# Optimization experiments

Hardware: AMD Instinct MI355X
Metric: run time of the kernel (lower is better)

## Reference

```python
import jax, jax.numpy as jnp
import numpy as np

DIM = 512
HEADS = 8
DIM_HEAD = 64
LANDMARKS = 256  # dim // 2
PINV_ITERS = 6
KERNEL = 33  # residual conv kernel
NUM_LAYERS = 2
NUM_CLASSES = 2


def layernorm(x, g, b, eps=1e-5):
    mu = x.mean(-1, keepdims=True)
    var = ((x - mu) ** 2).mean(-1, keepdims=True)
    return (x - mu) * jax.lax.rsqrt(var + eps) * g + b


def moore_penrose_pinv(x, iters=PINV_ITERS):
    # x: (b, h, m, m); scaling uses GLOBAL max over all batch/heads (torch.max)
    abs_x = jnp.abs(x)
    col = abs_x.sum(-1).max()
    row = abs_x.sum(-2).max()
    z = jnp.swapaxes(x, -1, -2) / (col * row)
    I = jnp.eye(x.shape[-1], dtype=x.dtype)
    for _ in range(iters):
        xz = x @ z
        z = 0.25 * z @ (13. * I - xz @ (15. * I - xz @ (7. * I - xz)))
    return z


def nystrom_attention(x, w_qkv, w_out, b_out, conv_w):
    # x: (b, n, dim)
    b, n, _ = x.shape
    m = LANDMARKS
    pad = (m - n % m) % m
    if pad:
        x = jnp.pad(x, ((0, 0), (pad, 0), (0, 0)))  # pad at FRONT
    nf = n + pad
    qkv = x @ w_qkv  # (b, nf, 3*h*dh)
    qkv = qkv.reshape(b, nf, 3, HEADS, DIM_HEAD)
    q = jnp.transpose(qkv[:, :, 0], (0, 2, 1, 3)) * (DIM_HEAD ** -0.5)  # (b,h,nf,dh)
    k = jnp.transpose(qkv[:, :, 1], (0, 2, 1, 3))
    v = jnp.transpose(qkv[:, :, 2], (0, 2, 1, 3))
    l = nf // m
    q_l = q.reshape(b, HEADS, m, l, DIM_HEAD).mean(3)  # (b,h,m,dh)
    k_l = k.reshape(b, HEADS, m, l, DIM_HEAD).mean(3)
    sim1 = jnp.einsum('bhid,bhjd->bhij', q, k_l)      # (b,h,nf,m)
    sim2 = jnp.einsum('bhid,bhjd->bhij', q_l, k_l)    # (b,h,m,m)
    sim3 = jnp.einsum('bhid,bhjd->bhij', q_l, k)      # (b,h,m,nf)
    attn1 = jax.nn.softmax(sim1, axis=-1)
    attn2 = jax.nn.softmax(sim2, axis=-1)
    attn3 = jax.nn.softmax(sim3, axis=-1)
    attn2_inv = moore_penrose_pinv(attn2)
    out = (attn1 @ attn2_inv) @ (attn3 @ v)  # (b,h,nf,dh)
    # residual depthwise conv over sequence dim, per head (Conv2d groups=heads)
    res = jax.lax.conv_general_dilated(
        v, conv_w, window_strides=(1, 1), padding=((KERNEL // 2, KERNEL // 2), (0, 0)),
        dimension_numbers=('NCHW', 'OIHW', 'NCHW'), feature_group_count=HEADS)
    out = out + res
    out = jnp.transpose(out, (0, 2, 1, 3)).reshape(b, nf, HEADS * DIM_HEAD)
    out = out @ w_out + b_out
    return out[:, -n:]


def setup_inputs() -> dict:
    key = jax.random.key(0)
    ks = jax.random.split(key, 16)
    B, N = 2, 8191
    s = 0.02
    inp = {
        'h': jax.random.normal(ks[0], (B, N, 1024), jnp.float32),
        'w1': jax.random.normal(ks[1], (1024, DIM), jnp.float32) * s,
        'b1': jnp.zeros((DIM,), jnp.float32),
        'cls_token': jax.random.normal(ks[2], (1, 1, DIM), jnp.float32),
        'ln_g': jnp.ones((NUM_LAYERS, DIM), jnp.float32),
        'ln_b': jnp.zeros((NUM_LAYERS, DIM), jnp.float32),
        'w_qkv': jax.random.normal(ks[3], (NUM_LAYERS, DIM, 3 * HEADS * DIM_HEAD), jnp.float32) * s,
        'w_out': jax.random.normal(ks[4], (NUM_LAYERS, HEADS * DIM_HEAD, DIM), jnp.float32) * s,
        'b_out': jnp.zeros((NUM_LAYERS, DIM), jnp.float32),
        'conv_w': jax.random.normal(ks[5], (NUM_LAYERS, HEADS, 1, KERNEL, 1), jnp.float32) * s,
        'fn_g': jnp.ones((DIM,), jnp.float32),
        'fn_b': jnp.zeros((DIM,), jnp.float32),
        'w2': jax.random.normal(ks[6], (DIM, NUM_CLASSES), jnp.float32) * s,
        'b2': jnp.zeros((NUM_CLASSES,), jnp.float32),
    }
    return inp


def reference(h, w1, b1, cls_token, ln_g, ln_b, w_qkv, w_out, b_out, conv_w, fn_g, fn_b, w2, b2):
    x = jax.nn.relu(h @ w1 + b1)  # (B,N,512)
    B = x.shape[0]
    cls = jnp.broadcast_to(cls_token, (B, 1, DIM))
    x = jnp.concatenate([cls, x], axis=1)  # (B, N+1, 512)
    for i in range(NUM_LAYERS):
        x = x + nystrom_attention(layernorm(x, ln_g[i], ln_b[i]), w_qkv[i], w_out[i], b_out[i], conv_w[i])
    x = layernorm(x, fn_g, fn_b)[:, 0]
    logits = x @ w2 + b2
    return logits
```

## Files before the change

### kernel.cpp

```cpp
#include <hip/hip_runtime.h>
#include <hip/hip_bf16.h>

#define DIM 512
#define HEADS 8
#define DH 64
#define LM 256
#define NF 8192
#define BHN 16

typedef __attribute__((ext_vector_type(8))) short short8;
typedef __attribute__((ext_vector_type(4))) float f32x4;

__device__ __forceinline__ float bf2f(unsigned short u) {
  return __uint_as_float((unsigned)u << 16);
}
__device__ __forceinline__ unsigned short f2bf(float x) {
  unsigned u = __float_as_uint(x);
  unsigned r = u + 0x7fffu + ((u >> 16) & 1u);
  return (unsigned short)(r >> 16);
}

__device__ __forceinline__ void gl2lds16(const void* g, void* l) {
  __builtin_amdgcn_global_load_lds(
      (const __attribute__((address_space(1))) void*)g,
      (__attribute__((address_space(3))) void*)l, 16, 0, 0);
}

__device__ __forceinline__ float waveReduceSum(float v) {
#pragma unroll
  for (int o = 1; o < 64; o <<= 1) v += __shfl_xor(v, o);
  return v;
}
__device__ __forceinline__ float waveReduceMax(float v) {
#pragma unroll
  for (int o = 1; o < 64; o <<= 1) v = fmaxf(v, __shfl_xor(v, o));
  return v;
}
__device__ __forceinline__ float blockReduceSum256(float v, float* sm) {
  v = waveReduceSum(v);
  int w = threadIdx.x >> 6;
  __syncthreads();
  if ((threadIdx.x & 63) == 0) sm[w] = v;
  __syncthreads();
  return sm[0] + sm[1] + sm[2] + sm[3];
}
__device__ __forceinline__ float blockReduceMax256(float v, float* sm) {
  v = waveReduceMax(v);
  int w = threadIdx.x >> 6;
  __syncthreads();
  if ((threadIdx.x & 63) == 0) sm[w] = v;
  __syncthreads();
  return fmaxf(fmaxf(sm[0], sm[1]), fmaxf(sm[2], sm[3]));
}

__global__ __launch_bounds__(256)
void cvt_bf16(const float* __restrict__ in, unsigned short* __restrict__ out,
              long long n) {
  long long i = ((long long)blockIdx.x * 256 + threadIdx.x) * 4;
  if (i + 3 < n) {
    float4 v = *(const float4*)&in[i];
    ushort4 o;
    o.x = f2bf(v.x); o.y = f2bf(v.y); o.z = f2bf(v.z); o.w = f2bf(v.w);
    *(ushort4*)&out[i] = o;
  } else {
    for (; i < n; i++) out[i] = f2bf(in[i]);
  }
}

__global__ __launch_bounds__(256)
void cvt_transpose(const float* __restrict__ in, unsigned short* __restrict__ out,
                   int Kd, int Nd) {
  __shared__ float t[32][33];
  int x = threadIdx.x & 31, y = threadIdx.x >> 5;
#pragma unroll
  for (int i = 0; i < 32; i += 8) {
    int k = blockIdx.y * 32 + y + i, n = blockIdx.x * 32 + x;
    t[y + i][x] = in[(long long)k * Nd + n];
  }
  __syncthreads();
#pragma unroll
  for (int i = 0; i < 32; i += 8) {
    int n = blockIdx.x * 32 + y + i, k = blockIdx.y * 32 + x;
    out[(long long)n * Kd + k] = f2bf(t[x][y + i]);
  }
}

__global__ __launch_bounds__(256)
void vt_transpose(const unsigned short* __restrict__ VB,
                  unsigned short* __restrict__ VT) {
  __shared__ unsigned short t[64][80];
  int bh = blockIdx.x >> 7, tile = blockIdx.x & 127;
  int n0 = tile * 64;
  int tid = threadIdx.x;
#pragma unroll
  for (int it = 0; it < 2; it++) {
    int s = it * 256 + tid;
    int nl = s >> 3, sg = s & 7;
    *(short8*)&t[nl][sg * 8] =
        *(const short8*)&VB[((long long)bh * NF + n0 + nl) * DH + sg * 8];
  }
  __syncthreads();
#pragma unroll
  for (int it = 0; it < 2; it++) {
    int s = it * 256 + tid;
    int dl = s >> 3, sg = s & 7;
    short8 v;
#pragma unroll
    for (int j = 0; j < 8; j++) ((unsigned short*)&v)[j] = t[sg * 8 + j][dl];
    *(short8*)&VT[((long long)bh * DH + dl) * NF + n0 + sg * 8] = v;
  }
}

__global__ __launch_bounds__(256) void zero_f(float* __restrict__ p, int n) {
  int i = blockIdx.x * 256 + threadIdx.x;
  if (i < n) p[i] = 0.f;
}

__global__ __launch_bounds__(256) void write_cls(const float* __restrict__ cls,
                                                 float* __restrict__ X) {
  int t = blockIdx.x * 256 + threadIdx.x;
  int b = t >> 9, c = t & 511;
  X[(long long)b * NF * DIM + c] = cls[c];
}

#define MG_RELU 1
#define MG_ADDC 2
#define MG_BIAS 4
__global__ __launch_bounds__(256)
void gemm_mfma(const unsigned short* __restrict__ A,
               const unsigned short* __restrict__ B,
               const float* __restrict__ bias, float* __restrict__ C,
               unsigned short* __restrict__ qkv, unsigned short* __restrict__ vbuf,
               int M, int N, int K, int flags, int remap) {
  __shared__ short8 smem[1024];
  short8 (*Als)[64] = (short8 (*)[64])smem;
  short8 (*Bls)[64] = (short8 (*)[64])(smem + 512);
  const int tid = threadIdx.x;
  const int lane = tid & 63, wave = tid >> 6;
  const int wm = wave >> 1, wn = wave & 1;
  const int m0 = blockIdx.y * 128, n0 = blockIdx.x * 128;
  const int r16 = lane & 15, quad = lane >> 4;
  const unsigned short* pa0 = A + (long long)(m0 + 32 * wave + r16) * K + quad * 8;
  const unsigned short* pa1 = A + (long long)(m0 + 32 * wave + 16 + r16) * K + quad * 8;
  const unsigned short* pb0 = B + (long long)(n0 + 32 * wave + r16) * K + quad * 8;
  const unsigned short* pb1 = B + (long long)(n0 + 32 * wave + 16 + r16) * K + quad * 8;
  f32x4 acc[4][4] = {};
  for (int k0 = 0; k0 < K; k0 += 32) {
    gl2lds16(pa0, &Als[2 * wave][0]);
    gl2lds16(pa1, &Als[2 * wave + 1][0]);
    gl2lds16(pb0, &Bls[2 * wave][0]);
    gl2lds16(pb1, &Bls[2 * wave + 1][0]);
    pa0 += 32; pa1 += 32; pb0 += 32; pb1 += 32;
    __syncthreads();
    short8 af[4], bfr[4];
#pragma unroll
    for (int mt = 0; mt < 4; mt++) af[mt] = Als[wm * 4 + mt][lane];
#pragma unroll
    for (int nt = 0; nt < 4; nt++) bfr[nt] = Bls[wn * 4 + nt][lane];
#pragma unroll
    for (int mt = 0; mt < 4; mt++)
#pragma unroll
      for (int nt = 0; nt < 4; nt++)
        acc[mt][nt] = __builtin_amdgcn_mfma_f32_16x16x32_bf16(
            af[mt], bfr[nt], acc[mt][nt], 0, 0, 0);
    __syncthreads();
  }
  if (remap == 2) {
    unsigned short (*Ep)[32][64] = (unsigned short (*)[32][64])smem;
    int gn_base = n0 + wn * 64;
    int s = gn_base >> 9, hh = (gn_base >> 6) & 7;
    float scale = (s == 0) ? 0.125f : 1.f;
    unsigned short* basep =
        (s == 0) ? qkv : (s == 1) ? qkv + (long long)BHN * NF * DH : vbuf;
#pragma unroll
    for (int half = 0; half < 2; half++) {
      __builtin_amdgcn_s_waitcnt(0);
#pragma unroll
      for (int mt = half * 2; mt < half * 2 + 2; mt++)
#pragma unroll
        for (int nt = 0; nt < 4; nt++)
#pragma unroll
          for (int r = 0; r < 4; r++)
            Ep[wave][(mt & 1) * 16 + quad * 4 + r][nt * 16 + r16] =
                f2bf(acc[mt][nt][r] * scale);
      __builtin_amdgcn_s_waitcnt(0);
#pragma unroll
      for (int it = 0; it < 4; it++) {
        int idx = it * 64 + lane;
        int m_l = idx >> 3, sg = idx & 7;
        int gm = m0 + wm * 64 + half * 32 + m_l;
        int b = gm >> 13, n = gm & (NF - 1);
        int bh = b * HEADS + hh;
        short8 v = *(short8*)&Ep[wave][m_l][sg * 8];
        *(short8*)&basep[((long long)bh * NF + n) * DH + sg * 8] = v;
      }
    }
  } else {
#pragma unroll
    for (int mt = 0; mt < 4; mt++) {
#pragma unroll
      for (int nt = 0; nt < 4; nt++) {
#pragma unroll
        for (int r = 0; r < 4; r++) {
          int gm = m0 + wm * 64 + mt * 16 + quad * 4 + r;
          int gn = n0 + wn * 64 + nt * 16 + r16;
          if (gm >= M) continue;
          float v = acc[mt][nt][r];
          if (flags & MG_BIAS) v += bias[gn];
          long long idx;
          if (remap == 1) {
            int b = gm / 8191;
            int n = gm - b * 8191;
            idx = ((long long)(b * NF + 1 + n)) * DIM + gn;
          } else {
            idx = (long long)gm * N + gn;
          }
          if (flags & MG_ADDC) v += C[idx];
          if (flags & MG_RELU) v = fmaxf(v, 0.f);
          C[idx] = v;
        }
      }
    }
  }
}

__global__ __launch_bounds__(256)
void flash_attn1(const unsigned short* __restrict__ QB,
                 const unsigned short* __restrict__ KLB,
                 const unsigned short* __restrict__ WmB,
                 const unsigned short* __restrict__ XNC,
                 unsigned short* __restrict__ XNB2) {
  __shared__ unsigned short Plds[4][16][264];
  const int bh = blockIdx.y, b = bh >> 3, hh = bh & 7;
  const int tid = threadIdx.x, lane = tid & 63, wave = tid >> 6;
  const int r16 = lane & 15, quad = lane >> 4;
  const int m0w = blockIdx.x * 64 + wave * 16;
  const unsigned short* Aq = QB + (long long)bh * NF * DH;
  const unsigned short* Bk = KLB + (long long)bh * LM * DH;
  short8 af[2];
#pragma unroll
  for (int kc = 0; kc < 2; kc++)
    af[kc] = *(const short8*)&Aq[(long long)(m0w + r16) * DH + kc * 32 + quad * 8];
  f32x4 S[16] = {};
#pragma unroll
  for (int nt = 0; nt < 16; nt++) {
#pragma unroll
    for (int kc = 0; kc < 2; kc++) {
      short8 bb = *(const short8*)&Bk[(long long)(nt * 16 + r16) * DH + kc * 32 + quad * 8];
      S[nt] = __builtin_amdgcn_mfma_f32_16x16x32_bf16(af[kc], bb, S[nt], 0, 0, 0);
    }
  }
  float inv[4];
#pragma unroll
  for (int r = 0; r < 4; r++) {
    float m_ = S[0][r];
#pragma unroll
    for (int nt = 1; nt < 16; nt++) m_ = fmaxf(m_, S[nt][r]);
#pragma unroll
    for (int o = 1; o < 16; o <<= 1) m_ = fmaxf(m_, __shfl_xor(m_, o));
    float s_ = 0.f;
#pragma unroll
    for (int nt = 0; nt < 16; nt++) {
      float e = __expf(S[nt][r] - m_);
      S[nt][r] = e;
      s_ += e;
    }
#pragma unroll
    for (int o = 1; o < 16; o <<= 1) s_ += __shfl_xor(s_, o);
    inv[r] = 1.f / s_;
  }
#pragma unroll
  for (int nt = 0; nt < 16; nt++)
#pragma unroll
    for (int r = 0; r < 4; r++)
      Plds[wave][quad * 4 + r][nt * 16 + r16] = f2bf(S[nt][r] * inv[r]);
  __builtin_amdgcn_s_waitcnt(0);
  f32x4 O[4] = {};
#pragma unroll
  for (int kc = 0; kc < 8; kc++) {
    short8 a = *(short8*)&Plds[wave][r16][kc * 32 + quad * 8];
#pragma unroll
    for (int nt2 = 0; nt2 < 4; nt2++) {
      short8 bb = *(const short8*)&WmB[((long long)bh * DH + nt2 * 16 + r16) * LM +
                                       kc * 32 + quad * 8];
      O[nt2] = __builtin_amdgcn_mfma_f32_16x16x32_bf16(a, bb, O[nt2], 0, 0, 0);
    }
  }
#pragma unroll
  for (int nt2 = 0; nt2 < 4; nt2++)
#pragma unroll
    for (int r = 0; r < 4; r++) {
      int row = m0w + quad * 4 + r;
      int d = nt2 * 16 + r16;
      long long gi = ((long long)(b * NF + row)) * DIM + hh * DH + d;
      XNB2[gi] = f2bf(O[nt2][r] + bf2f(XNC[gi]));
    }
}

__global__ __launch_bounds__(256)
void flash_attn3(const unsigned short* __restrict__ QLB,
                 const unsigned short* __restrict__ KB,
                 const unsigned short* __restrict__ VT,
                 float* __restrict__ Opart, float* __restrict__ Mpart,
                 float* __restrict__ Lpart) {
  __shared__ unsigned short Plds[4][16][136];
  const int bh = blockIdx.z, ks = blockIdx.y;
  const int tid = threadIdx.x, lane = tid & 63, wave = tid >> 6;
  const int r16 = lane & 15, quad = lane >> 4;
  const int m0w = blockIdx.x * 64 + wave * 16;
  const unsigned short* Aq = QLB + (long long)bh * LM * DH;
  const unsigned short* Bk = KB + (long long)bh * NF * DH;
  const unsigned short* Vt = VT + (long long)bh * DH * NF;
  short8 af[2];
#pragma unroll
  for (int kc = 0; kc < 2; kc++)
    af[kc] = *(const short8*)&Aq[(long long)(m0w + r16) * DH + kc * 32 + quad * 8];
  f32x4 O[4] = {};
  float rm[4] = {-1e30f, -1e30f, -1e30f, -1e30f};
  float rl[4] = {};
  for (int t = 0; t < 4; t++) {
    int kv0 = ks * 512 + t * 128;
    f32x4 S[8] = {};
#pragma unroll
    for (int nt = 0; nt < 8; nt++) {
#pragma unroll
      for (int kc = 0; kc < 2; kc++) {
        short8 bb = *(const short8*)&Bk[(long long)(kv0 + nt * 16 + r16) * DH +
                                        kc * 32 + quad * 8];
        S[nt] = __builtin_amdgcn_mfma_f32_16x16x32_bf16(af[kc], bb, S[nt], 0, 0, 0);
      }
    }
#pragma unroll
    for (int r = 0; r < 4; r++) {
      float mt = S[0][r];
#pragma unroll
      for (int nt = 1; nt < 8; nt++) mt = fmaxf(mt, S[nt][r]);
#pragma unroll
      for (int o = 1; o < 16; o <<= 1) mt = fmaxf(mt, __shfl_xor(mt, o));
      float nm = fmaxf(rm[r], mt);
      float al = __expf(rm[r] - nm);
      rm[r] = nm;
      float s_ = 0.f;
#pragma unroll
      for (int nt = 0; nt < 8; nt++) {
        float e = __expf(S[nt][r] - nm);
        S[nt][r] = e;
        s_ += e;
      }
#pragma unroll
      for (int o = 1; o < 16; o <<= 1) s_ += __shfl_xor(s_, o);
      rl[r] = rl[r] * al + s_;
#pragma unroll
      for (int nt2 = 0; nt2 < 4; nt2++) O[nt2][r] *= al;
    }
#pragma unroll
    for (int nt = 0; nt < 8; nt++)
#pragma unroll
      for (int r = 0; r < 4; r++)
        Plds[wave][quad * 4 + r][nt * 16 + r16] = f2bf(S[nt][r]);
    __builtin_amdgcn_s_waitcnt(0);
#pragma unroll
    for (int kc2 = 0; kc2 < 4; kc2++) {
      short8 a = *(short8*)&Plds[wave][r16][kc2 * 32 + quad * 8];
#pragma unroll
      for (int nt2 = 0; nt2 < 4; nt2++) {
        short8 bb = *(const short8*)&Vt[(long long)(nt2 * 16 + r16) * NF + kv0 +
                                        kc2 * 32 + quad * 8];
        O[nt2] = __builtin_amdgcn_mfma_f32_16x16x32_bf16(a, bb, O[nt2], 0, 0, 0);
      }
    }
  }
  float* Ob = Opart + (((long long)ks * BHN + bh) * LM) * DH;
#pragma unroll
  for (int nt2 = 0; nt2 < 4; nt2++)
#pragma unroll
    for (int r = 0; r < 4; r++) {
      int row = m0w + quad * 4 + r;
      Ob[(long long)row * DH + nt2 * 16 + r16] = O[nt2][r];
    }
  if (r16 == 0) {
#pragma unroll
    for (int r = 0; r < 4; r++) {
      int row = m0w + quad * 4 + r;
      Mpart[((long long)ks * BHN + bh) * LM + row] = rm[r];
      Lpart[((long long)ks * BHN + bh) * LM + row] = rl[r];
    }
  }
}

__global__ __launch_bounds__(256)
void attn3_merge(const float* __restrict__ Opart, const float* __restrict__ Mpart,
                 const float* __restrict__ Lpart, float* __restrict__ O3) {
  int idx = blockIdx.x * 256 + threadIdx.x;
  int bh = idx >> 14, rem = idx & 16383;
  int row = rem >> 6, d = rem & 63;
  float mg = -1e30f;
#pragma unroll
  for (int c = 0; c < 16; c++)
    mg = fmaxf(mg, Mpart[((long long)c * BHN + bh) * LM + row]);
  float L = 0.f, acc = 0.f;
#pragma unroll
  for (int c = 0; c < 16; c++) {
    float e = __expf(Mpart[((long long)c * BHN + bh) * LM + row] - mg);
    L += Lpart[((long long)c * BHN + bh) * LM + row] * e;
    acc += Opart[(((long long)c * BHN + bh) * LM + row) * DH + d] * e;
  }
  O3[((long long)bh * LM + row) * DH + d] = acc / L;
}

__global__ __launch_bounds__(256)
void zinit(const float* __restrict__ a2, const unsigned* __restrict__ red,
           unsigned short* __restrict__ zn, unsigned short* __restrict__ zt) {
  float scale = 1.0f / __uint_as_float(red[1]);
  long long idx = (long long)blockIdx.x * 256 + threadIdx.x;
  int bh = (int)(idx >> 16);
  int ij = (int)(idx & 65535);
  int i = ij >> 8, j = ij & 255;
  zn[idx] = f2bf(a2[((long long)bh << 16) + (j << 8) + i] * scale);
  zt[idx] = f2bf(a2[idx] * scale);
}

#define PV_CN 1
#define PV_CT 2
#define PV_CF 4
#define PV_ID 8
__global__ __launch_bounds__(256)
void pinv_bf(const unsigned short* __restrict__ An,
             const unsigned short* __restrict__ Bt,
             unsigned short* __restrict__ Cn, unsigned short* __restrict__ Ct,
             float* __restrict__ Cf, float alpha, float ident, float beta,
             int flags) {
  __shared__ unsigned short Als[64][256];
  __shared__ unsigned short Bls[64][256];
  const int batch = blockIdx.z;
  An += (long long)batch * 65536;
  Bt += (long long)batch * 65536;
  const int tid = threadIdx.x, lane = tid & 63, wave = tid >> 6;
  const int wm2 = wave >> 1, wn2 = wave & 1;
  const int m0 = blockIdx.y * 64, n0 = blockIdx.x * 64;
  const int r16 = lane & 15, quad = lane >> 4;
#pragma unroll
  for (int j = 0; j < 8; j++) {
    int g = (j * 4 + wave) * 64 + lane;
    int row = g >> 5, plog = (g & 31) ^ (row & 7);
    gl2lds16(An + ((m0 + row) << 8) + plog * 8,
             (char*)Als + (j * 4 + wave) * 1024);
    gl2lds16(Bt + ((n0 + row) << 8) + plog * 8,
             (char*)Bls + (j * 4 + wave) * 1024);
  }
  __syncthreads();
  f32x4 acc[2][2] = {};
  const int arow0 = wm2 * 32 + r16, brow0 = wn2 * 32 + r16;
#pragma unroll
  for (int kk = 0; kk < 8; kk++) {
    short8 af[2], bfr[2];
#pragma unroll
    for (int mt = 0; mt < 2; mt++) {
      int row = arow0 + mt * 16;
      af[mt] = *(const short8*)((const char*)Als + row * 512 +
                                ((kk * 4 + quad) ^ (row & 7)) * 16);
    }
#pragma unroll
    for (int nt = 0; nt < 2; nt++) {
      int row = brow0 + nt * 16;
      bfr[nt] = *(const short8*)((const char*)Bls + row * 512 +
                                 ((kk * 4 + quad) ^ (row & 7)) * 16);
    }
#pragma unroll
    for (int mt = 0; mt < 2; mt++)
#pragma unroll
      for (int nt = 0; nt < 2; nt++)
        acc[mt][nt] = __builtin_amdgcn_mfma_f32_16x16x32_bf16(
            af[mt], bfr[nt], acc[mt][nt], 0, 0, 0);
  }
  long long cb = (long long)batch * 65536;
#pragma unroll
  for (int mt = 0; mt < 2; mt++) {
#pragma unroll
    for (int nt = 0; nt < 2; nt++) {
      int ncol = n0 + wn2 * 32 + nt * 16 + r16;
      float vals[4];
#pragma unroll
      for (int r = 0; r < 4; r++) {
        int mrow = wm2 * 32 + mt * 16 + quad * 4 + r;
        float v = beta * acc[mt][nt][r];
        if (flags & PV_ID) {
          unsigned short a = *(const unsigned short*)(
              (const char*)Als + mrow * 512 +
              (((ncol >> 3) ^ (mrow & 7)) * 16) + (ncol & 7) * 2);
          v += ident * bf2f(a);
        }
        vals[r] = v * alpha;
        int gm = m0 + mrow;
        if (flags & PV_CN) Cn[cb + ((long long)gm << 8) + ncol] = f2bf(vals[r]);
        if (flags & PV_CF) Cf[cb + ((long long)gm << 8) + ncol] = vals[r];
      }
      if (flags & PV_CT) {
        ushort4 o;
        o.x = f2bf(vals[0]); o.y = f2bf(vals[1]);
        o.z = f2bf(vals[2]); o.w = f2bf(vals[3]);
        *(ushort4*)&Ct[cb + ((long long)ncol << 8) + m0 + wm2 * 32 + mt * 16 +
                       quad * 4] = o;
      }
    }
  }
}

#define BG_BIDENT 16
__global__ __launch_bounds__(256)
void bgemm(const float* __restrict__ A, const float* __restrict__ B,
           float* __restrict__ C, int M, int N, int K,
           long long sA, long long sB, long long sC,
           float alpha, float ident, int flags) {
  const int batch = blockIdx.z;
  A += (long long)batch * sA;
  B += (long long)batch * sB;
  float* Cb = C + (long long)batch * sC;
  __shared__ float As[16][68];
  __shared__ float Bs[16][68];
  const int tid = threadIdx.x;
  const int tx = tid & 15, ty = tid >> 4;
  const int m0 = blockIdx.y * 64, n0 = blockIdx.x * 64;
  float acc[4][4] = {};
  for (int k0 = 0; k0 < K; k0 += 16) {
    {
      int k = tid & 15;
      int mBase = tid >> 4;
#pragma unroll
      for (int i = 0; i < 4; i++) {
        int m = mBase + i * 16;
        int gm = m0 + m;
        As[k][m] = (gm < M) ? A[(long long)gm * K + (k0 + k)] : 0.f;
      }
    }
    {
      int n = tid & 63;
      int kBase = tid >> 6;
#pragma unroll
      for (int i = 0; i < 4; i++) {
        int k = kBase + i * 4;
        int gn = n0 + n;
        float vb = (gn < N) ? B[(long long)(k0 + k) * N + gn] : 0.f;
        if (flags & BG_BIDENT) vb = ident * ((k0 + k) == gn ? 1.f : 0.f) - vb;
        Bs[k][n] = vb;
      }
    }
    __syncthreads();
#pragma unroll
    for (int k = 0; k < 16; k++) {
      float a[4], b[4];
#pragma unroll
      for (int i = 0; i < 4; i++) a[i] = As[k][ty * 4 + i];
#pragma unroll
      for (int j = 0; j < 4; j++) b[j] = Bs[k][tx * 4 + j];
#pragma unroll
      for (int i = 0; i < 4; i++)
#pragma unroll
        for (int j = 0; j < 4; j++) acc[i][j] = fmaf(a[i], b[j], acc[i][j]);
    }
    __syncthreads();
  }
#pragma unroll
  for (int i = 0; i < 4; i++) {
    int gm = m0 + ty * 4 + i;
    if (gm >= M) continue;
#pragma unroll
    for (int j = 0; j < 4; j++) {
      int gn = n0 + tx * 4 + j;
      if (gn >= N) continue;
      Cb[(long long)gm * N + gn] = alpha * acc[i][j];
    }
  }
}

__global__ __launch_bounds__(256)
void wm_gemm(const float* __restrict__ Z, const float* __restrict__ O3,
             unsigned short* __restrict__ WmT) {
  const int batch = blockIdx.y;
  const int m0 = blockIdx.x * 64;
  const float* A = Z + (long long)batch * 65536;
  const float* B = O3 + (long long)batch * LM * DH;
  __shared__ float As[16][68];
  __shared__ float Bs[16][68];
  const int tid = threadIdx.x, tx = tid & 15, ty = tid >> 4;
  float acc[4][4] = {};
  for (int k0 = 0; k0 < 256; k0 += 16) {
    {
      int k = tid & 15, mB = tid >> 4;
#pragma unroll
      for (int i = 0; i < 4; i++) {
        int m = mB + i * 16;
        As[k][m] = A[(long long)(m0 + m) * 256 + k0 + k];
      }
    }
    {
      int n = tid & 63, kB = tid >> 6;
#pragma unroll
      for (int i = 0; i < 4; i++) {
        int k = kB + i * 4;
        Bs[k][n] = B[(long long)(k0 + k) * DH + n];
      }
    }
    __syncthreads();
#pragma unroll
    for (int k = 0; k < 16; k++) {
      float a[4], b[4];
#pragma unroll
      for (int i = 0; i < 4; i++) a[i] = As[k][ty * 4 + i];
#pragma unroll
      for (int j = 0; j < 4; j++) b[j] = Bs[k][tx * 4 + j];
#pragma unroll
      for (int i = 0; i < 4; i++)
#pragma unroll
        for (int j = 0; j < 4; j++) acc[i][j] = fmaf(a[i], b[j], acc[i][j]);
    }
    __syncthreads();
  }
#pragma unroll
  for (int i = 0; i < 4; i++)
#pragma unroll
    for (int j = 0; j < 4; j++)
      WmT[((long long)batch * DH + tx * 4 + j) * LM + m0 + ty * 4 + i] =
          f2bf(acc[i][j]);
}

__global__ __launch_bounds__(256)
void layernorm_rows_bf16(const float* __restrict__ X, const float* __restrict__ g,
                         const float* __restrict__ bt,
                         unsigned short* __restrict__ Y) {
  __shared__ float sm[4];
  long long r = blockIdx.x;
  const float* x = X + r * DIM;
  int t = threadIdx.x;
  float v0 = x[t], v1 = x[t + 256];
  float mu = blockReduceSum256(v0 + v1, sm) * (1.f / DIM);
  float d0 = v0 - mu, d1 = v1 - mu;
  float var = blockReduceSum256(d0 * d0 + d1 * d1, sm) * (1.f / DIM);
  float rs = 1.0f / sqrtf(var + 1e-5f);
  unsigned short* y = Y + r * DIM;
  y[t] = f2bf(d0 * rs * g[t] + bt[t]);
  y[t + 256] = f2bf(d1 * rs * g[t + 256] + bt[t + 256]);
}

__global__ __launch_bounds__(64)
void landmarks_k(const unsigned short* __restrict__ q,
                 const unsigned short* __restrict__ k,
                 float* __restrict__ ql, float* __restrict__ kl,
                 unsigned short* __restrict__ qlb,
                 unsigned short* __restrict__ klb) {
  int bh = blockIdx.x >> 8, i = blockIdx.x & 255, d = threadIdx.x;
  long long base = ((long long)bh * NF + i * 32) * DH + d;
  float sq = 0.f, sk = 0.f;
#pragma unroll 4
  for (int l = 0; l < 32; l++) {
    sq += bf2f(q[base + (long long)l * DH]);
    sk += bf2f(k[base + (long long)l * DH]);
  }
  long long o = ((long long)bh * LM + i) * DH + d;
  float mq = sq * (1.f / 32.f), mk = sk * (1.f / 32.f);
  ql[o] = mq; kl[o] = mk;
  qlb[o] = f2bf(mq); klb[o] = f2bf(mk);
}

__global__ __launch_bounds__(256)
void sim2_softmax(const float* __restrict__ ql, const float* __restrict__ kl,
                  float* __restrict__ a2, unsigned short* __restrict__ a2b) {
  __shared__ float qs[64];
  __shared__ float sm[4];
  int bh = blockIdx.x >> 8, i = blockIdx.x & 255, t = threadIdx.x;
  if (t < 64) qs[t] = ql[((long long)bh * LM + i) * DH + t];
  __syncthreads();
  const float* krow = kl + (long long)bh * LM * DH + (long long)t * DH;
  float s = 0.f;
#pragma unroll
  for (int d = 0; d < 64; d++) s += qs[d] * krow[d];
  float m = blockReduceMax256(s, sm);
  float e = expf(s - m);
  float sum = blockReduceSum256(e, sm);
  long long off = ((long long)bh * LM + i) * LM + t;
  float v = e / sum;
  a2[off] = v;
  a2b[off] = f2bf(v);
}

__global__ __launch_bounds__(256)
void pinv_reduce(const float* __restrict__ a2, unsigned* __restrict__ red) {
  __shared__ float sm[4];
  int bh = blockIdx.x, t = threadIdx.x;
  const float* A = a2 + (long long)bh * LM * LM;
  float cs = 0.f;
  for (int i = 0; i < 256; i++) cs += fabsf(A[i * 256 + t]);
  float cm = blockReduceMax256(cs, sm);
  if (t == 0) atomicMax(&red[1], __float_as_uint(cm));
}

__global__ __launch_bounds__(256)
void conv_res_bf16(const unsigned short* __restrict__ vt,
                   const float* __restrict__ cw,
                   unsigned short* __restrict__ out) {
  int bh = blockIdx.x >> 6, tile = blockIdx.x & 63;
  int b = bh >> 3, hh = bh & 7;
  int t = threadIdx.x;
  int d = t & 63, pg = t >> 6;
  float wr[33];
#pragma unroll
  for (int kk = 0; kk < 33; kk++) wr[kk] = cw[hh * 33 + kk];
  const unsigned short* src = &vt[((long long)bh * DH + d) * NF];
  int base = tile * 128 + pg * 32;
  int n0 = base - 16;
  float win[64];
#pragma unroll
  for (int jj = 0; jj < 8; jj++) {
    int c = n0 + jj * 8;
    if (c >= 0 && c + 7 < NF) {
      short8 v = *(const short8*)&src[c];
#pragma unroll
      for (int j = 0; j < 8; j++)
        win[jj * 8 + j] = bf2f((unsigned short)v[j]);
    } else {
#pragma unroll
      for (int j = 0; j < 8; j++) {
        int nn = c + j;
        win[jj * 8 + j] = (nn >= 0 && nn < NF) ? bf2f(src[nn]) : 0.f;
      }
    }
  }
  unsigned short* dst = &out[((long long)(b * NF + base)) * DIM + hh * DH + d];
#pragma unroll
  for (int p = 0; p < 32; p++) {
    float s = 0.f;
#pragma unroll
    for (int kk = 0; kk < 33; kk++) s = fmaf(wr[kk], win[p + kk], s);
    dst[(long long)p * DIM] = f2bf(s);
  }
}

__global__ __launch_bounds__(256)
void final_head(const float* __restrict__ X, const float* __restrict__ g,
                const float* __restrict__ bt, const float* __restrict__ w2,
                const float* __restrict__ b2, float* __restrict__ out) {
  __shared__ float sm[4];
  int b = blockIdx.x, t = threadIdx.x;
  const float* row = X + (long long)b * NF * DIM;
  float v0 = row[t], v1 = row[t + 256];
  float mu = blockReduceSum256(v0 + v1, sm) * (1.f / DIM);
  float d0 = v0 - mu, d1 = v1 - mu;
  float var = blockReduceSum256(d0 * d0 + d1 * d1, sm) * (1.f / DIM);
  float rs = 1.0f / sqrtf(var + 1e-5f);
  float y0 = d0 * rs * g[t] + bt[t];
  float y1 = d1 * rs * g[t + 256] + bt[t + 256];
  float l0 = y0 * w2[t * 2 + 0] + y1 * w2[(t + 256) * 2 + 0];
  float l1 = y0 * w2[t * 2 + 1] + y1 * w2[(t + 256) * 2 + 1];
  l0 = blockReduceSum256(l0, sm);
  l1 = blockReduceSum256(l1, sm);
  if (t == 0) {
    out[b * 2 + 0] = l0 + b2[0];
    out[b * 2 + 1] = l1 + b2[1];
  }
}

extern "C" void kernel_launch(void* const* d_in, const int* in_sizes, int n_in,
                              void* d_out, int out_size, void* d_ws,
                              size_t ws_size, hipStream_t stream) {
  const float* h      = (const float*)d_in[0];
  const float* w1     = (const float*)d_in[1];
  const float* b1     = (const float*)d_in[2];
  const float* cls    = (const float*)d_in[3];
  const float* ln_g   = (const float*)d_in[4];
  const float* ln_b   = (const float*)d_in[5];
  const float* w_qkv  = (const float*)d_in[6];
  const float* w_out  = (const float*)d_in[7];
  const float* b_out  = (const float*)d_in[8];
  const float* conv_w = (const float*)d_in[9];
  const float* fn_g   = (const float*)d_in[10];
  const float* fn_b   = (const float*)d_in[11];
  const float* w2     = (const float*)d_in[12];
  const float* b2     = (const float*)d_in[13];

  float* ws = (float*)d_ws;
  const long long XSZ = (long long)2 * NF * DIM;
  const long long QSZ = (long long)BHN * NF * DH;
  float* X  = ws;
  unsigned short* STAGE = (unsigned short*)(X + XSZ);
  unsigned short* HB   = STAGE;
  unsigned short* XNB1 = STAGE;
  unsigned short* XNB2 = STAGE;
  unsigned short* VB   = STAGE + XSZ;
  unsigned short* XNC  = STAGE + XSZ;
  unsigned short* QB = STAGE + 2 * XSZ;
  unsigned short* KB = QB + QSZ;
  unsigned short* VT = KB + QSZ;
  float* QL = (float*)(VT + QSZ);
  float* KL = QL + 262144;
  unsigned short* QLB = (unsigned short*)(KL + 262144);
  unsigned short* KLB = QLB + 262144;
  float* A2 = (float*)(KLB + 262144);
  float* ZA = A2 + 1048576;
  float* ZB = ZA + 1048576;
  float* P  = ZB + 1048576;
  float* T1 = P + 1048576;
  float* T2 = T1 + 1048576;
  float* Mpart = T2 + 1048576;
  float* Lpart = Mpart + 65536;
  float* O3 = Lpart + 65536;
  unsigned short* WmB = (unsigned short*)(O3 + 262144);
  unsigned* RED = (unsigned*)(WmB + 262144);
  unsigned short* WT = (unsigned short*)(RED + 4);
  unsigned short* W1T = WT;
  unsigned short* WQ0 = W1T + 524288;
  unsigned short* WQ1 = WQ0 + 786432;
  unsigned short* WO0 = WQ1 + 786432;
  unsigned short* WO1 = WO0 + 262144;

  unsigned short* A2B = VB;
  float* Opart = (float*)VB;
  unsigned short* Zan = (unsigned short*)P;
  unsigned short* Zat = Zan + 1048576;
  unsigned short* Zbn = (unsigned short*)ZB;
  unsigned short* Zbt = Zbn + 1048576;
  unsigned short* Pn  = (unsigned short*)T1;
  unsigned short* Pt  = Pn + 1048576;
  unsigned short* T1t = (unsigned short*)T2;
  unsigned short* T2t = T1t + 1048576;

  write_cls<<<4, 256, 0, stream>>>(cls, X);
  cvt_bf16<<<16382, 256, 0, stream>>>(h, HB, (long long)16382 * 1024);
  cvt_transpose<<<dim3(512 / 32, 1024 / 32), 256, 0, stream>>>(w1, W1T, 1024, 512);
  cvt_transpose<<<dim3(1536 / 32, 512 / 32), 256, 0, stream>>>(w_qkv, WQ0, 512, 1536);
  cvt_transpose<<<dim3(1536 / 32, 512 / 32), 256, 0, stream>>>(
      w_qkv + (long long)DIM * 1536, WQ1, 512, 1536);
  cvt_transpose<<<dim3(512 / 32, 512 / 32), 256, 0, stream>>>(w_out, WO0, 512, 512);
  cvt_transpose<<<dim3(512 / 32, 512 / 32), 256, 0, stream>>>(
      w_out + (long long)DIM * DIM, WO1, 512, 512);
  gemm_mfma<<<dim3(4, 128), 256, 0, stream>>>(HB, W1T, b1, X, nullptr, nullptr,
                                              16382, 512, 1024, MG_RELU | MG_BIAS, 1);

  for (int L = 0; L < 2; L++) {
    layernorm_rows_bf16<<<2 * NF, 256, 0, stream>>>(X, ln_g + L * DIM,
                                                    ln_b + L * DIM, XNB1);
    gemm_mfma<<<dim3(12, 128), 256, 0, stream>>>(XNB1, L ? WQ1 : WQ0, nullptr,
                                                 nullptr, QB, VB, 16384, 1536,
                                                 512, 0, 2);
    vt_transpose<<<BHN * 128, 256, 0, stream>>>(VB, VT);

    landmarks_k<<<BHN * LM, 64, 0, stream>>>(QB, KB, QL, KL, QLB, KLB);
    sim2_softmax<<<BHN * LM, 256, 0, stream>>>(QL, KL, A2, A2B);
    zero_f<<<1, 256, 0, stream>>>((float*)RED, 4);
    pinv_reduce<<<BHN, 256, 0, stream>>>(A2, RED);
    zinit<<<4096, 256, 0, stream>>>(A2, RED, Zan, Zat);
    for (int it = 0; it < 5; it++) {
      const unsigned short* zcn = (it & 1) ? Zbn : Zan;
      const unsigned short* zct = (it & 1) ? Zbt : Zat;
      unsigned short* znn = (it & 1) ? Zan : Zbn;
      unsigned short* znt = (it & 1) ? Zat : Zbt;
      pinv_bf<<<dim3(4, 4, BHN), 256, 0, stream>>>(
          A2B, zct, Pn, Pt, nullptr, 1.f, 0.f, 1.f, PV_CN | PV_CT);
      pinv_bf<<<dim3(4, 4, BHN), 256, 0, stream>>>(
          Pn, Pt, nullptr, T1t, nullptr, 1.f, 7.f, -1.f, PV_CT | PV_ID);
      pinv_bf<<<dim3(4, 4, BHN), 256, 0, stream>>>(
          Pn, T1t, nullptr, T2t, nullptr, 1.f, 15.f, -1.f, PV_CT | PV_ID);
      if (it < 4)
        pinv_bf<<<dim3(4, 4, BHN), 256, 0, stream>>>(
            zcn, T2t, znn, znt, nullptr, 0.25f, 13.f, -1.f,
            PV_CN | PV_CT | PV_ID);
      else
        pinv_bf<<<dim3(4, 4, BHN), 256, 0, stream>>>(
            zcn, T2t, nullptr, nullptr, ZB, 0.25f, 13.f, -1.f, PV_CF | PV_ID);
    }
    bgemm<<<dim3(4, 4, BHN), 256, 0, stream>>>(A2, ZB, P, 256, 256, 256,
                                               65536, 65536, 65536, 1.f, 0.f, 0);
    bgemm<<<dim3(4, 4, BHN), 256, 0, stream>>>(P, P, T1, 256, 256, 256,
                                               65536, 65536, 65536, 1.f, 7.f,
                                               BG_BIDENT);
    bgemm<<<dim3(4, 4, BHN), 256, 0, stream>>>(P, T1, T2, 256, 256, 256,
                                               65536, 65536, 65536, 1.f, 15.f,
                                               BG_BIDENT);
    bgemm<<<dim3(4, 4, BHN), 256, 0, stream>>>(ZB, T2, ZA, 256, 256, 256,
                                               65536, 65536, 65536, 0.25f,
                                               13.f, BG_BIDENT);

    flash_attn3<<<dim3(4, 16, BHN), 256, 0, stream>>>(QLB, KB, VT, Opart, Mpart,
                                                      Lpart);
    attn3_merge<<<1024, 256, 0, stream>>>(Opart, Mpart, Lpart, O3);

    wm_gemm<<<dim3(4, BHN), 256, 0, stream>>>(ZA, O3, WmB);

    conv_res_bf16<<<BHN * 64, 256, 0, stream>>>(VT, conv_w + L * 264, XNC);

    flash_attn1<<<dim3(128, BHN), 256, 0, stream>>>(QB, KLB, WmB, XNC, XNB2);

    gemm_mfma<<<dim3(4, 128), 256, 0, stream>>>(XNB2, L ? WO1 : WO0,
                                                b_out + L * DIM, X, nullptr,
                                                nullptr, 16384, 512, 512,
                                                MG_ADDC | MG_BIAS, 0);
  }
  final_head<<<2, 256, 0, stream>>>(X, fn_g, fn_b, w2, b2, (float*)d_out);
}
```

Before: 1.440 ms.

## Shrink pinv tiles to 32x32, halve attn1 LDS staging, add MFMA priority hints

The pinv_bf batched GEMM now uses 32x32 output tiles with one MFMA accumulator per wave, launched on an 8x8 grid, giving four times as many blocks for the small 256x256 per-head matmuls. Each block also stages only 32 rows of A and B in LDS. flash_attn1 writes the softmax probabilities to LDS in two halves of 128 columns, halving its shared buffer. s_setprio is raised around the MFMA loops in both attention kernels. The aim is more occupancy and parallelism for the pinv chain and better interleaving of matrix and other work. The cost is less data reuse per block in pinv and an extra wait/LDS round in attn1.

```diff
diff --git a/kernel.cpp b/kernel.cpp
--- a/kernel.cpp
+++ b/kernel.cpp
@@ -230,7 +230,7 @@
                  const unsigned short* __restrict__ WmB,
                  const unsigned short* __restrict__ XNC,
                  unsigned short* __restrict__ XNB2) {
-  __shared__ unsigned short Plds[4][16][264];
+  __shared__ unsigned short Plds[4][16][136];
   const int bh = blockIdx.y, b = bh >> 3, hh = bh & 7;
   const int tid = threadIdx.x, lane = tid & 63, wave = tid >> 6;
   const int r16 = lane & 15, quad = lane >> 4;
@@ -242,6 +242,7 @@
   for (int kc = 0; kc < 2; kc++)
     af[kc] = *(const short8*)&Aq[(long long)(m0w + r16) * DH + kc * 32 + quad * 8];
   f32x4 S[16] = {};
+  __builtin_amdgcn_s_setprio(1);
 #pragma unroll
   for (int nt = 0; nt < 16; nt++) {
 #pragma unroll
@@ -250,6 +251,7 @@
       S[nt] = __builtin_amdgcn_mfma_f32_16x16x32_bf16(af[kc], bb, S[nt], 0, 0, 0);
     }
   }
+  __builtin_amdgcn_s_setprio(0);
   float inv[4];
 #pragma unroll
   for (int r = 0; r < 4; r++) {
@@ -269,22 +271,28 @@
     for (int o = 1; o < 16; o <<= 1) s_ += __shfl_xor(s_, o);
     inv[r] = 1.f / s_;
   }
-#pragma unroll
-  for (int nt = 0; nt < 16; nt++)
-#pragma unroll
-    for (int r = 0; r < 4; r++)
-      Plds[wave][quad * 4 + r][nt * 16 + r16] = f2bf(S[nt][r] * inv[r]);
-  __builtin_amdgcn_s_waitcnt(0);
   f32x4 O[4] = {};
 #pragma unroll
-  for (int kc = 0; kc < 8; kc++) {
-    short8 a = *(short8*)&Plds[wave][r16][kc * 32 + quad * 8];
-#pragma unroll
-    for (int nt2 = 0; nt2 < 4; nt2++) {
-      short8 bb = *(const short8*)&WmB[((long long)bh * DH + nt2 * 16 + r16) * LM +
-                                       kc * 32 + quad * 8];
-      O[nt2] = __builtin_amdgcn_mfma_f32_16x16x32_bf16(a, bb, O[nt2], 0, 0, 0);
-    }
+  for (int half = 0; half < 2; half++) {
+#pragma unroll
+    for (int nt = 0; nt < 8; nt++)
+#pragma unroll
+      for (int r = 0; r < 4; r++)
+        Plds[wave][quad * 4 + r][nt * 16 + r16] =
+            f2bf(S[half * 8 + nt][r] * inv[r]);
+    __builtin_amdgcn_s_waitcnt(0);
+    __builtin_amdgcn_s_setprio(1);
+#pragma unroll
+    for (int kc = 0; kc < 4; kc++) {
+      short8 a = *(short8*)&Plds[wave][r16][kc * 32 + quad * 8];
+#pragma unroll
+      for (int nt2 = 0; nt2 < 4; nt2++) {
+        short8 bb = *(const short8*)&WmB[((long long)bh * DH + nt2 * 16 + r16) * LM +
+                                         half * 128 + kc * 32 + quad * 8];
+        O[nt2] = __builtin_amdgcn_mfma_f32_16x16x32_bf16(a, bb, O[nt2], 0, 0, 0);
+      }
+    }
+    __builtin_amdgcn_s_setprio(0);
   }
 #pragma unroll
   for (int nt2 = 0; nt2 < 4; nt2++)
@@ -321,6 +329,7 @@
   for (int t = 0; t < 4; t++) {
     int kv0 = ks * 512 + t * 128;
     f32x4 S[8] = {};
+    __builtin_amdgcn_s_setprio(1);
 #pragma unroll
     for (int nt = 0; nt < 8; nt++) {
 #pragma unroll
@@ -330,6 +339,7 @@
         S[nt] = __builtin_amdgcn_mfma_f32_16x16x32_bf16(af[kc], bb, S[nt], 0, 0, 0);
       }
     }
+    __builtin_amdgcn_s_setprio(0);
 #pragma unroll
     for (int r = 0; r < 4; r++) {
       float mt = S[0][r];
@@ -359,6 +369,7 @@
       for (int r = 0; r < 4; r++)
         Plds[wave][quad * 4 + r][nt * 16 + r16] = f2bf(S[nt][r]);
     __builtin_amdgcn_s_waitcnt(0);
+    __builtin_amdgcn_s_setprio(1);
 #pragma unroll
     for (int kc2 = 0; kc2 < 4; kc2++) {
       short8 a = *(short8*)&Plds[wave][r16][kc2 * 32 + quad * 8];
@@ -369,6 +380,7 @@
         O[nt2] = __builtin_amdgcn_mfma_f32_16x16x32_bf16(a, bb, O[nt2], 0, 0, 0);
       }
     }
+    __builtin_amdgcn_s_setprio(0);
   }
   float* Ob = Opart + (((long long)ks * BHN + bh) * LM) * DH;
 #pragma unroll
@@ -430,17 +442,17 @@
              unsigned short* __restrict__ Cn, unsigned short* __restrict__ Ct,
              float* __restrict__ Cf, float alpha, float ident, float beta,
              int flags) {
-  __shared__ unsigned short Als[64][256];
-  __shared__ unsigned short Bls[64][256];
+  __shared__ unsigned short Als[32][256];
+  __shared__ unsigned short Bls[32][256];
   const int batch = blockIdx.z;
   An += (long long)batch * 65536;
   Bt += (long long)batch * 65536;
   const int tid = threadIdx.x, lane = tid & 63, wave = tid >> 6;
   const int wm2 = wave >> 1, wn2 = wave & 1;
-  const int m0 = blockIdx.y * 64, n0 = blockIdx.x * 64;
+  const int m0 = blockIdx.y * 32, n0 = blockIdx.x * 32;
   const int r16 = lane & 15, quad = lane >> 4;
 #pragma unroll
-  for (int j = 0; j < 8; j++) {
+  for (int j = 0; j < 4; j++) {
     int g = (j * 4 + wave) * 64 + lane;
     int row = g >> 5, plog = (g & 31) ^ (row & 7);
     gl2lds16(An + ((m0 + row) << 8) + plog * 8,
@@ -449,60 +461,39 @@
              (char*)Bls + (j * 4 + wave) * 1024);
   }
   __syncthreads();
-  f32x4 acc[2][2] = {};
-  const int arow0 = wm2 * 32 + r16, brow0 = wn2 * 32 + r16;
+  f32x4 acc = {};
+  const int arow = wm2 * 16 + r16, brow = wn2 * 16 + r16;
 #pragma unroll
   for (int kk = 0; kk < 8; kk++) {
-    short8 af[2], bfr[2];
-#pragma unroll
-    for (int mt = 0; mt < 2; mt++) {
-      int row = arow0 + mt * 16;
-      af[mt] = *(const short8*)((const char*)Als + row * 512 +
-                                ((kk * 4 + quad) ^ (row & 7)) * 16);
-    }
-#pragma unroll
-    for (int nt = 0; nt < 2; nt++) {
-      int row = brow0 + nt * 16;
-      bfr[nt] = *(const short8*)((const char*)Bls + row * 512 +
-                                 ((kk * 4 + quad) ^ (row & 7)) * 16);
-    }
-#pragma unroll
-    for (int mt = 0; mt < 2; mt++)
-#pragma unroll
-      for (int nt = 0; nt < 2; nt++)
-        acc[mt][nt] = __builtin_amdgcn_mfma_f32_16x16x32_bf16(
-            af[mt], bfr[nt], acc[mt][nt], 0, 0, 0);
+    short8 af = *(const short8*)((const char*)Als + arow * 512 +
+                                 ((kk * 4 + quad) ^ (arow & 7)) * 16);
+    short8 bfr = *(const short8*)((const char*)Bls + brow * 512 +
+                                  ((kk * 4 + quad) ^ (brow & 7)) * 16);
+    acc = __builtin_amdgcn_mfma_f32_16x16x32_bf16(af, bfr, acc, 0, 0, 0);
   }
   long long cb = (long long)batch * 65536;
-#pragma unroll
-  for (int mt = 0; mt < 2; mt++) {
-#pragma unroll
-    for (int nt = 0; nt < 2; nt++) {
-      int ncol = n0 + wn2 * 32 + nt * 16 + r16;
-      float vals[4];
-#pragma unroll
-      for (int r = 0; r < 4; r++) {
-        int mrow = wm2 * 32 + mt * 16 + quad * 4 + r;
-        float v = beta * acc[mt][nt][r];
-        if (flags & PV_ID) {
-          unsigned short a = *(const unsigned short*)(
-              (const char*)Als + mrow * 512 +
-              (((ncol >> 3) ^ (mrow & 7)) * 16) + (ncol & 7) * 2);
-          v += ident * bf2f(a);
-        }
-        vals[r] = v * alpha;
-        int gm = m0 + mrow;
-        if (flags & PV_CN) Cn[cb + ((long long)gm << 8) + ncol] = f2bf(vals[r]);
-        if (flags & PV_CF) Cf[cb + ((long long)gm << 8) + ncol] = vals[r];
-      }
-      if (flags & PV_CT) {
-        ushort4 o;
-        o.x = f2bf(vals[0]); o.y = f2bf(vals[1]);
-        o.z = f2bf(vals[2]); o.w = f2bf(vals[3]);
-        *(ushort4*)&Ct[cb + ((long long)ncol << 8) + m0 + wm2 * 32 + mt * 16 +
-                       quad * 4] = o;
-      }
-    }
+  int ncol = n0 + wn2 * 16 + r16;
+  float vals[4];
+#pragma unroll
+  for (int r = 0; r < 4; r++) {
+    int mrow = wm2 * 16 + quad * 4 + r;
+    float v = beta * acc[r];
+    if (flags & PV_ID) {
+      unsigned short a = *(const unsigned short*)(
+          (const char*)Als + mrow * 512 +
+          (((ncol >> 3) ^ (mrow & 7)) * 16) + (ncol & 7) * 2);
+      v += ident * bf2f(a);
+    }
+    vals[r] = v * alpha;
+    int gm = m0 + mrow;
+    if (flags & PV_CN) Cn[cb + ((long long)gm << 8) + ncol] = f2bf(vals[r]);
+    if (flags & PV_CF) Cf[cb + ((long long)gm << 8) + ncol] = vals[r];
+  }
+  if (flags & PV_CT) {
+    ushort4 o;
+    o.x = f2bf(vals[0]); o.y = f2bf(vals[1]);
+    o.z = f2bf(vals[2]); o.w = f2bf(vals[3]);
+    *(ushort4*)&Ct[cb + ((long long)ncol << 8) + m0 + wm2 * 16 + quad * 4] = o;
   }
 }
 
@@ -853,18 +844,18 @@
       const unsigned short* zct = (it & 1) ? Zbt : Zat;
       unsigned short* znn = (it & 1) ? Zan : Zbn;
       unsigned short* znt = (it & 1) ? Zat : Zbt;
-      pinv_bf<<<dim3(4, 4, BHN), 256, 0, stream>>>(
+      pinv_bf<<<dim3(8, 8, BHN), 256, 0, stream>>>(
           A2B, zct, Pn, Pt, nullptr, 1.f, 0.f, 1.f, PV_CN | PV_CT);
-      pinv_bf<<<dim3(4, 4, BHN), 256, 0, stream>>>(
+      pinv_bf<<<dim3(8, 8, BHN), 256, 0, stream>>>(
           Pn, Pt, nullptr, T1t, nullptr, 1.f, 7.f, -1.f, PV_CT | PV_ID);
-      pinv_bf<<<dim3(4, 4, BHN), 256, 0, stream>>>(
+      pinv_bf<<<dim3(8, 8, BHN), 256, 0, stream>>>(
           Pn, T1t, nullptr, T2t, nullptr, 1.f, 15.f, -1.f, PV_CT | PV_ID);
       if (it < 4)
-        pinv_bf<<<dim3(4, 4, BHN), 256, 0, stream>>>(
+        pinv_bf<<<dim3(8, 8, BHN), 256, 0, stream>>>(
             zcn, T2t, znn, znt, nullptr, 0.25f, 13.f, -1.f,
             PV_CN | PV_CT | PV_ID);
       else
-        pinv_bf<<<dim3(4, 4, BHN), 256, 0, stream>>>(
+        pinv_bf<<<dim3(8, 8, BHN), 256, 0, stream>>>(
             zcn, T2t, nullptr, nullptr, ZB, 0.25f, 13.f, -1.f, PV_CF | PV_ID);
     }
     bgemm<<<dim3(4, 4, BHN), 256, 0, stream>>>(A2, ZB, P, 256, 256, 256,
```

After: 1.464 ms. About the same (+1.7%).
